# Kernel tuning notes

Hardware: AMD Instinct MI355X
Metric: run time of the kernel (lower is better)

The kernel has to match this reference:

```python
import jax, jax.numpy as jnp
import numpy as np

# --- config (Qwen3-Next linear attention defaults) ---
B, S, H = 1, 256, 2048
NK, NV, DK, DV, K = 4, 32, 128, 128, 4
KEY_DIM = NK * DK          # 512
VAL_DIM = NV * DV          # 4096
CONV_DIM = 2 * KEY_DIM + VAL_DIM  # 5120
EPS = 1e-6


def setup_inputs() -> dict:
    key = jax.random.key(0)
    ks = jax.random.split(key, 8)
    rn = lambda k, shape, sc: jax.random.normal(k, shape, jnp.float32) * sc
    return {
        "hidden_states": jax.random.normal(ks[0], (B, S, H), jnp.float32),
        "w_qkvz": rn(ks[1], (2 * KEY_DIM + 2 * VAL_DIM, H), 0.02),  # in_proj_qkvz weight
        "w_ba": rn(ks[2], (2 * NV, H), 0.02),                        # in_proj_ba weight
        "w_out": rn(ks[3], (H, VAL_DIM), 0.02),                      # out_proj weight
        "conv_w": rn(ks[4], (CONV_DIM, 1, K), 0.1),                  # depthwise conv weight [C,1,K]
        "dt_bias": jnp.ones((NV,), jnp.float32),
        "A_log": jnp.zeros((NV,), jnp.float32),
        "norm_w": jnp.ones((DV,), jnp.float32),
    }


def reference(hidden_states, w_qkvz, w_ba, w_out, conv_w, dt_bias, A_log, norm_w):
    b, s, _ = hidden_states.shape
    # input projections (Linear without bias: x @ W.T)
    qkvz = hidden_states @ w_qkvz.T                      # [B,S,9216]
    ba = hidden_states @ w_ba.T                          # [B,S,64]
    q, k, v, z = jnp.split(qkvz, [KEY_DIM, 2 * KEY_DIM, 2 * KEY_DIM + VAL_DIM], axis=-1)
    beta, alpha = jnp.split(ba, 2, axis=-1)              # each [B,S,NV]

    # causal depthwise conv over concat(q,k,v), then silu
    qkv = jnp.concatenate([q, k, v], axis=-1).transpose(0, 2, 1)   # [B,C,S]
    qkv = jax.lax.conv_general_dilated(
        qkv, conv_w, window_strides=(1,), padding=[(K - 1, 0)],
        dimension_numbers=("NCH", "OIH", "NCH"), feature_group_count=CONV_DIM)
    qkv = jax.nn.silu(qkv).transpose(0, 2, 1)            # [B,S,C]
    q, k, v = jnp.split(qkv, [KEY_DIM, 2 * KEY_DIM], axis=-1)

    q = q.reshape(b, s, NK, DK)
    k = k.reshape(b, s, NK, DK)
    v = v.reshape(b, s, NV, DV)
    z = z.reshape(b, s, NV, DV)

    # GQA-style head expansion (repeat_interleave)
    ratio = NV // NK
    q = jnp.repeat(q, ratio, axis=2)                     # [B,S,NV,DK]
    k = jnp.repeat(k, ratio, axis=2)

    # NOTE: original computes g = -softplus(-A_log - alpha) but never uses it (dead code).
    beta_g = jax.nn.sigmoid(beta + dt_bias)[..., None]   # [B,S,NV,1]
    q = q * (DK ** -0.5)

    # naive delta-rule: full outer-product tensor + cumsum (memory-bound)
    kv = jnp.einsum("bsnk,bsnv->bsnkv", k, v * beta_g)   # [B,S,NV,DK,DV]
    out = jnp.einsum("bsnk,bsnkv->bsnv", q, jnp.cumsum(kv, axis=1))  # [B,S,NV,DV]

    # gated RMSNorm over head_v_dim in fp32
    of = out.astype(jnp.float32)
    var = jnp.mean(of * of, axis=-1, keepdims=True)
    of = of * jax.lax.rsqrt(var + EPS) * norm_w
    of = of * jax.nn.silu(z.astype(jnp.float32))

    return of.reshape(b, s, VAL_DIM) @ w_out.T           # [B,S,H]
```

## Files before the change

### kernel.cpp

```cpp
#include <hip/hip_runtime.h>
#include <hip/hip_bf16.h>

#define S_LEN   256
#define HID     2048
#define NVH     32
#define DKD     128
#define DVD     128
#define KEYDIM  512
#define VALDIM  4096
#define CONVDIM 5120
#define QKVZ_N  9216
#define EPS_F   1e-6f

typedef __attribute__((ext_vector_type(8))) short bf16x8;
typedef __attribute__((ext_vector_type(4))) float f32x4;

__device__ __forceinline__ unsigned short f2bf(float f) {
    union { float f; unsigned int i; } v; v.f = f;
    unsigned int x = v.i;
    return (unsigned short)((x + 0x7FFFu + ((x >> 16) & 1u)) >> 16);
}
__device__ __forceinline__ unsigned int pk2(float x, float y) {
    union { __hip_bfloat162 h; unsigned int u; } c;
    c.h = __float22bfloat162_rn(float2{x, y});
    return c.u;
}
__device__ __forceinline__ float4 asf4(uint4 u) {
    union { uint4 u; float4 f; } c; c.u = u; return c.f;
}
__device__ __forceinline__ uint4 cvt8_pack(float4 a, float4 b) {
    uint4 r;
    r.x = pk2(a.x, a.y); r.y = pk2(a.z, a.w);
    r.z = pk2(b.x, b.y); r.w = pk2(b.z, b.w);
    return r;
}

template<bool A_F32>
__global__ __launch_bounds__(256, 2)
void gemm_tile(const void* __restrict__ Ap, const float* __restrict__ B,
               float* __restrict__ Cpart, int N, int K, int kc) {
    __shared__ __align__(16) unsigned short As[128][72];
    __shared__ __align__(16) unsigned short Bs[128][72];

    const int tid  = threadIdx.x;
    const int lane = tid & 63, wave = tid >> 6;
    const int wm = wave >> 1, wn = wave & 1;
    const int quad = lane >> 4, l16 = lane & 15;
    const int m0 = blockIdx.y * 128, n0 = blockIdx.x * 128;
    const int kbeg = blockIdx.z * kc;
    const int niter = kc >> 6;

    const int lc = (tid & 7) << 3;
    const int lr = tid >> 3;

    f32x4 acc[4][4];
#pragma unroll
    for (int i = 0; i < 4; i++)
#pragma unroll
        for (int j = 0; j < 4; j++) acc[i][j] = (f32x4){0.f, 0.f, 0.f, 0.f};

    uint4 qa[8], qb[8];

    auto ld_tiles = [&](int kk) {
        if constexpr (A_F32) {
            const float* a = (const float*)Ap + (size_t)(m0 + lr) * K + kk + lc;
#pragma unroll
            for (int i = 0; i < 4; i++) {
                qa[2 * i]     = *(const uint4*)(a + (size_t)(32 * i) * K);
                qa[2 * i + 1] = *(const uint4*)(a + (size_t)(32 * i) * K + 4);
            }
        } else {
            const unsigned short* a = (const unsigned short*)Ap + (size_t)(m0 + lr) * K + kk + lc;
#pragma unroll
            for (int i = 0; i < 4; i++)
                qa[i] = *(const uint4*)(a + (size_t)(32 * i) * K);
        }
        const float* b = B + (size_t)(n0 + lr) * K + kk + lc;
#pragma unroll
        for (int i = 0; i < 4; i++) {
            qb[2 * i]     = *(const uint4*)(b + (size_t)(32 * i) * K);
            qb[2 * i + 1] = *(const uint4*)(b + (size_t)(32 * i) * K + 4);
        }
    };
    auto st_tiles = [&]() {
#pragma unroll
        for (int i = 0; i < 4; i++) {
            if constexpr (A_F32)
                *(uint4*)(&As[lr + 32 * i][lc]) = cvt8_pack(asf4(qa[2 * i]), asf4(qa[2 * i + 1]));
            else
                *(uint4*)(&As[lr + 32 * i][lc]) = qa[i];
            *(uint4*)(&Bs[lr + 32 * i][lc]) = cvt8_pack(asf4(qb[2 * i]), asf4(qb[2 * i + 1]));
        }
    };

    ld_tiles(kbeg);
    st_tiles();
    __syncthreads();

    for (int it = 0; it < niter; ++it) {
        if (it + 1 < niter) ld_tiles(kbeg + (it + 1) * 64);

        bf16x8 af[2][4], bfr[2][4];
#pragma unroll
        for (int t = 0; t < 4; t++) {
#pragma unroll
            for (int ks = 0; ks < 2; ks++) {
                af[ks][t]  = *(const bf16x8*)(&As[wm * 64 + t * 16 + l16][ks * 32 + quad * 8]);
                bfr[ks][t] = *(const bf16x8*)(&Bs[wn * 64 + t * 16 + l16][ks * 32 + quad * 8]);
            }
        }
#pragma unroll
        for (int ks = 0; ks < 2; ks++)
#pragma unroll
            for (int i = 0; i < 4; i++)
#pragma unroll
                for (int j = 0; j < 4; j++)
                    acc[i][j] = __builtin_amdgcn_mfma_f32_16x16x32_bf16(af[ks][i], bfr[ks][j], acc[i][j], 0, 0, 0);

        if (it + 1 < niter) {
            __syncthreads();
            st_tiles();
            __syncthreads();
        }
    }

    float* C = Cpart + (size_t)blockIdx.z * 256 * N;
#pragma unroll
    for (int i = 0; i < 4; i++)
#pragma unroll
        for (int j = 0; j < 4; j++)
#pragma unroll
            for (int r = 0; r < 4; r++) {
                int row = m0 + wm * 64 + i * 16 + quad * 4 + r;
                int col = n0 + wn * 64 + j * 16 + l16;
                C[(size_t)row * N + col] = acc[i][j][r];
            }
}

template<int P>
__global__ void reduce_sum(const float* __restrict__ part, float* __restrict__ out, int n) {
    int i = (blockIdx.x * 256 + threadIdx.x) * 4;
    if (i >= n) return;
    float4 s = *(const float4*)(part + i);
#pragma unroll
    for (int p = 1; p < P; p++) {
        float4 v = *(const float4*)(part + (size_t)p * n + i);
        s.x += v.x; s.y += v.y; s.z += v.z; s.w += v.w;
    }
    *(float4*)(out + i) = s;
}

__global__ __launch_bounds__(256)
void ba_proj(const float* __restrict__ hs,
             const float* __restrict__ w_ba,
             float* __restrict__ ba) {
    int s = blockIdx.x;
    int n = threadIdx.x & 63, seg = threadIdx.x >> 6;
    const float* x = hs + (size_t)s * HID + seg * 512;
    const float* w = w_ba + (size_t)n * HID + seg * 512;
    float acc = 0.f;
#pragma unroll 4
    for (int k = 0; k < 512; k += 4) {
        float4 xv = *(const float4*)(x + k);
        float4 wv = *(const float4*)(w + k);
        acc += xv.x * wv.x + xv.y * wv.y + xv.z * wv.z + xv.w * wv.w;
    }
    __shared__ float parts[4][64];
    parts[seg][n] = acc;
    __syncthreads();
    if (threadIdx.x < 64)
        ba[s * 64 + threadIdx.x] = parts[0][threadIdx.x] + parts[1][threadIdx.x]
                                 + parts[2][threadIdx.x] + parts[3][threadIdx.x];
}

__global__ void conv_silu(const float* __restrict__ qkvz,
                          const float* __restrict__ conv_w,
                          float* __restrict__ out) {
    int idx = blockIdx.x * blockDim.x + threadIdx.x;
    if (idx >= S_LEN * CONVDIM) return;
    int s = idx / CONVDIM, c = idx % CONVDIM;
    float acc = 0.f;
#pragma unroll
    for (int j = 0; j < 4; j++) {
        int t = s - 3 + j;
        if (t >= 0) acc += qkvz[(size_t)t * QKVZ_N + c] * conv_w[c * 4 + j];
    }
    out[idx] = acc / (1.f + __expf(-acc));
}

__global__ __launch_bounds__(256)
void scores_k(const float* __restrict__ conv, const float* __restrict__ ba,
              const float* __restrict__ dt_bias, float* __restrict__ scores) {
    if (blockIdx.x > blockIdx.y) return;
    int hk = blockIdx.z;
    int s0 = blockIdx.y * 16, t0 = blockIdx.x * 16;
    __shared__ float Qs[16][132], Ks[16][132];
    int tid = threadIdx.x;
    int qoff = hk * DKD;
    int koff = KEYDIM + hk * DKD;
    for (int idx = tid; idx < 16 * 128; idx += 256) {
        int i = idx >> 7, d = idx & 127;
        Qs[i][d] = conv[(size_t)(s0 + i) * CONVDIM + qoff + d];
        Ks[i][d] = conv[(size_t)(t0 + i) * CONVDIM + koff + d];
    }
    __syncthreads();
    int tx = tid & 15, ty = tid >> 4;
    int s = s0 + ty, t = t0 + tx;
    float dot = 0.f;
    for (int d = 0; d < 128; d++) dot += Qs[ty][d] * Ks[tx][d];
    float base = (t <= s) ? dot * 0.08838834764831845f : 0.f;
#pragma unroll
    for (int v = 0; v < 8; v++) {
        int n = hk * 8 + v;
        float b = ba[t * 64 + n] + dt_bias[n];
        float bg = 1.f / (1.f + __expf(-b));
        scores[((size_t)n * 256 + s) * 256 + t] = base * bg;
    }
}

__global__ __launch_bounds__(256)
void attn_v(const float* __restrict__ scores, const float* __restrict__ conv,
            float* __restrict__ attn) {
    int n = blockIdx.y, s0 = blockIdx.x * 16;
    int voff = 2 * KEYDIM + n * DVD;
    __shared__ float Ss[16][17];
    __shared__ float Vs[16][132];
    int tid = threadIdx.x, sy = tid >> 4, dx = tid & 15;
    float acc[8] = {0.f, 0.f, 0.f, 0.f, 0.f, 0.f, 0.f, 0.f};
    for (int t0 = 0; t0 <= s0; t0 += 16) {
        Ss[sy][dx] = scores[((size_t)n * 256 + s0 + sy) * 256 + t0 + dx];
        const float* vp = conv + (size_t)(t0 + sy) * CONVDIM + voff + dx * 8;
        *(float4*)&Vs[sy][dx * 8]     = *(const float4*)vp;
        *(float4*)&Vs[sy][dx * 8 + 4] = *(const float4*)(vp + 4);
        __syncthreads();
#pragma unroll
        for (int j = 0; j < 16; j++) {
            float sv = Ss[sy][j];
#pragma unroll
            for (int r = 0; r < 8; r++) acc[r] += sv * Vs[j][dx + 16 * r];
        }
        __syncthreads();
    }
    float* op = attn + ((size_t)(s0 + sy) * NVH + n) * DVD;
#pragma unroll
    for (int r = 0; r < 8; r++) op[dx + 16 * r] = acc[r];
}

__global__ __launch_bounds__(128)
void rmsnorm_gate(const float* __restrict__ attn, const float* __restrict__ qkvz,
                  const float* __restrict__ norm_w,
                  unsigned short* __restrict__ normed) {
    int s = blockIdx.x >> 5, n = blockIdx.x & 31;
    int d = threadIdx.x;
    float x = attn[((size_t)s * NVH + n) * DVD + d];
    float sq = x * x;
#pragma unroll
    for (int off = 32; off > 0; off >>= 1) sq += __shfl_down(sq, off, 64);
    __shared__ float parts[2];
    if ((d & 63) == 0) parts[d >> 6] = sq;
    __syncthreads();
    float ms = (parts[0] + parts[1]) * (1.f / 128.f);
    float inv = rsqrtf(ms + EPS_F);
    float z = qkvz[(size_t)s * QKVZ_N + CONVDIM + n * DVD + d];
    float sz = z / (1.f + __expf(-z));
    float v = x * inv * norm_w[d] * sz;
    normed[((size_t)s * NVH + n) * DVD + d] = f2bf(v);
}

extern "C" void kernel_launch(void* const* d_in, const int* in_sizes, int n_in,
                              void* d_out, int out_size, void* d_ws, size_t ws_size,
                              hipStream_t stream) {
    const float* hs      = (const float*)d_in[0];
    const float* w_qkvz  = (const float*)d_in[1];
    const float* w_ba    = (const float*)d_in[2];
    const float* w_out   = (const float*)d_in[3];
    const float* conv_w  = (const float*)d_in[4];
    const float* dt_bias = (const float*)d_in[5];
    const float* norm_w  = (const float*)d_in[7];

    char* ws = (char*)d_ws;
    float* qkvz = (float*)ws;  ws += (size_t)S_LEN * QKVZ_N * 4;
    float* ba   = (float*)ws;  ws += (size_t)S_LEN * 64 * 4;
    float* conv = (float*)ws;  ws += (size_t)S_LEN * CONVDIM * 4;
    char* regB = ws;
    float* scratch1 = (float*)regB;
    unsigned short* normed = (unsigned short*)regB;
    float* scratch2 = (float*)(regB + 2097152);
    float* attn   = (float*)(regB + 2097152);
    float* scores = (float*)(regB + 2097152 + 4194304);

    const bool big = ws_size >= (size_t)54 * 1024 * 1024;
    const int sk1 = big ? 4 : 2;
    const int sk2 = big ? 16 : 8;

    gemm_tile<true><<<dim3(QKVZ_N / 128, 2, sk1), 256, 0, stream>>>(hs, w_qkvz, scratch1, QKVZ_N, HID, HID / sk1);
    ba_proj<<<S_LEN, 256, 0, stream>>>(hs, w_ba, ba);
    if (big) reduce_sum<4><<<(S_LEN * QKVZ_N) / 1024, 256, 0, stream>>>(scratch1, qkvz, S_LEN * QKVZ_N);
    else     reduce_sum<2><<<(S_LEN * QKVZ_N) / 1024, 256, 0, stream>>>(scratch1, qkvz, S_LEN * QKVZ_N);
    conv_silu<<<(S_LEN * CONVDIM) / 256, 256, 0, stream>>>(qkvz, conv_w, conv);
    scores_k<<<dim3(16, 16, 4), 256, 0, stream>>>(conv, ba, dt_bias, scores);
    attn_v<<<dim3(16, NVH), 256, 0, stream>>>(scores, conv, attn);
    rmsnorm_gate<<<S_LEN * NVH, 128, 0, stream>>>(attn, qkvz, norm_w, normed);
    gemm_tile<false><<<dim3(HID / 128, 2, sk2), 256, 0, stream>>>(normed, w_out, scratch2, HID, VALDIM, VALDIM / sk2);
    if (big) reduce_sum<16><<<(S_LEN * HID) / 1024, 256, 0, stream>>>(scratch2, (float*)d_out, S_LEN * HID);
    else     reduce_sum<8><<<(S_LEN * HID) / 1024, 256, 0, stream>>>(scratch2, (float*)d_out, S_LEN * HID);
}
```

Before: 274.5 us.

## Fuse attention pipeline, fold split-K reduction into conv, retile GEMM to 256x64

Several changes land together. The hidden states are converted to bf16 inside ba_proj, the GEMM is retiled to cover all 256 rows with 64-column tiles, and the first split-K reduction is folded into the conv kernel and the z read. scores_k, attn_v and rmsnorm_gate are fused into one attention kernel, which drops the scores and attn intermediates. The point is fewer launches and less intermediate global traffic. The cost is that the fused attention kernel recomputes QK per value head instead of sharing it per key head, and the workspace is now assumed large enough (about 45MB) with no fallback.

```diff
diff --git a/kernel.cpp b/kernel.cpp
--- a/kernel.cpp
+++ b/kernel.cpp
@@ -4,8 +4,6 @@
 #define S_LEN   256
 #define HID     2048
 #define NVH     32
-#define DKD     128
-#define DVD     128
 #define KEYDIM  512
 #define VALDIM  4096
 #define CONVDIM 5120
@@ -34,24 +32,23 @@
     r.z = pk2(b.x, b.y); r.w = pk2(b.z, b.w);
     return r;
 }
-
-template<bool A_F32>
-__global__ __launch_bounds__(256, 2)
-void gemm_tile(const void* __restrict__ Ap, const float* __restrict__ B,
+__device__ __forceinline__ float sigmoidf(float x) { return 1.f / (1.f + __expf(-x)); }
+
+__global__ __launch_bounds__(256, 3)
+void gemm_tile(const unsigned short* __restrict__ A, const float* __restrict__ B,
                float* __restrict__ Cpart, int N, int K, int kc) {
-    __shared__ __align__(16) unsigned short As[128][72];
-    __shared__ __align__(16) unsigned short Bs[128][72];
+    __shared__ __align__(16) unsigned short As[256][72];
+    __shared__ __align__(16) unsigned short Bs[64][72];
 
     const int tid  = threadIdx.x;
     const int lane = tid & 63, wave = tid >> 6;
-    const int wm = wave >> 1, wn = wave & 1;
     const int quad = lane >> 4, l16 = lane & 15;
-    const int m0 = blockIdx.y * 128, n0 = blockIdx.x * 128;
+    const int n0   = blockIdx.x * 64;
     const int kbeg = blockIdx.z * kc;
     const int niter = kc >> 6;
 
-    const int lc = (tid & 7) << 3;
-    const int lr = tid >> 3;
+    const int ar = tid >> 2;
+    const int ac = (tid & 3) << 4;
 
     f32x4 acc[4][4];
 #pragma unroll
@@ -59,38 +56,26 @@
 #pragma unroll
         for (int j = 0; j < 4; j++) acc[i][j] = (f32x4){0.f, 0.f, 0.f, 0.f};
 
-    uint4 qa[8], qb[8];
-
+    uint4 qa[8], qb[4];
     auto ld_tiles = [&](int kk) {
-        if constexpr (A_F32) {
-            const float* a = (const float*)Ap + (size_t)(m0 + lr) * K + kk + lc;
-#pragma unroll
-            for (int i = 0; i < 4; i++) {
-                qa[2 * i]     = *(const uint4*)(a + (size_t)(32 * i) * K);
-                qa[2 * i + 1] = *(const uint4*)(a + (size_t)(32 * i) * K + 4);
-            }
-        } else {
-            const unsigned short* a = (const unsigned short*)Ap + (size_t)(m0 + lr) * K + kk + lc;
-#pragma unroll
-            for (int i = 0; i < 4; i++)
-                qa[i] = *(const uint4*)(a + (size_t)(32 * i) * K);
-        }
-        const float* b = B + (size_t)(n0 + lr) * K + kk + lc;
-#pragma unroll
-        for (int i = 0; i < 4; i++) {
-            qb[2 * i]     = *(const uint4*)(b + (size_t)(32 * i) * K);
-            qb[2 * i + 1] = *(const uint4*)(b + (size_t)(32 * i) * K + 4);
-        }
+#pragma unroll
+        for (int p = 0; p < 4; p++) {
+            const unsigned short* a = A + (size_t)(ar + 64 * p) * K + kk + ac;
+            qa[2 * p]     = *(const uint4*)a;
+            qa[2 * p + 1] = *(const uint4*)(a + 8);
+        }
+        const float* b = B + (size_t)(n0 + ar) * K + kk + ac;
+#pragma unroll
+        for (int i = 0; i < 4; i++) qb[i] = *(const uint4*)(b + 4 * i);
     };
     auto st_tiles = [&]() {
 #pragma unroll
-        for (int i = 0; i < 4; i++) {
-            if constexpr (A_F32)
-                *(uint4*)(&As[lr + 32 * i][lc]) = cvt8_pack(asf4(qa[2 * i]), asf4(qa[2 * i + 1]));
-            else
-                *(uint4*)(&As[lr + 32 * i][lc]) = qa[i];
-            *(uint4*)(&Bs[lr + 32 * i][lc]) = cvt8_pack(asf4(qb[2 * i]), asf4(qb[2 * i + 1]));
-        }
+        for (int p = 0; p < 4; p++) {
+            *(uint4*)(&As[ar + 64 * p][ac])     = qa[2 * p];
+            *(uint4*)(&As[ar + 64 * p][ac + 8]) = qa[2 * p + 1];
+        }
+        *(uint4*)(&Bs[ar][ac])     = cvt8_pack(asf4(qb[0]), asf4(qb[1]));
+        *(uint4*)(&Bs[ar][ac + 8]) = cvt8_pack(asf4(qb[2]), asf4(qb[3]));
     };
 
     ld_tiles(kbeg);
@@ -105,8 +90,8 @@
         for (int t = 0; t < 4; t++) {
 #pragma unroll
             for (int ks = 0; ks < 2; ks++) {
-                af[ks][t]  = *(const bf16x8*)(&As[wm * 64 + t * 16 + l16][ks * 32 + quad * 8]);
-                bfr[ks][t] = *(const bf16x8*)(&Bs[wn * 64 + t * 16 + l16][ks * 32 + quad * 8]);
+                af[ks][t]  = *(const bf16x8*)(&As[wave * 64 + t * 16 + l16][ks * 32 + quad * 8]);
+                bfr[ks][t] = *(const bf16x8*)(&Bs[t * 16 + l16][ks * 32 + quad * 8]);
             }
         }
 #pragma unroll
@@ -131,8 +116,8 @@
         for (int j = 0; j < 4; j++)
 #pragma unroll
             for (int r = 0; r < 4; r++) {
-                int row = m0 + wm * 64 + i * 16 + quad * 4 + r;
-                int col = n0 + wn * 64 + j * 16 + l16;
+                int row = wave * 64 + i * 16 + quad * 4 + r;
+                int col = n0 + j * 16 + l16;
                 C[(size_t)row * N + col] = acc[i][j][r];
             }
 }
@@ -153,7 +138,8 @@
 __global__ __launch_bounds__(256)
 void ba_proj(const float* __restrict__ hs,
              const float* __restrict__ w_ba,
-             float* __restrict__ ba) {
+             float* __restrict__ ba,
+             unsigned short* __restrict__ hs_bf) {
     int s = blockIdx.x;
     int n = threadIdx.x & 63, seg = threadIdx.x >> 6;
     const float* x = hs + (size_t)s * HID + seg * 512;
@@ -167,72 +153,72 @@
     }
     __shared__ float parts[4][64];
     parts[seg][n] = acc;
+    int c = threadIdx.x * 8;
+    float4 h0 = *(const float4*)(hs + (size_t)s * HID + c);
+    float4 h1 = *(const float4*)(hs + (size_t)s * HID + c + 4);
+    *(uint4*)(hs_bf + (size_t)s * HID + c) = cvt8_pack(h0, h1);
     __syncthreads();
     if (threadIdx.x < 64)
         ba[s * 64 + threadIdx.x] = parts[0][threadIdx.x] + parts[1][threadIdx.x]
                                  + parts[2][threadIdx.x] + parts[3][threadIdx.x];
 }
 
-__global__ void conv_silu(const float* __restrict__ qkvz,
+__global__ void conv_red4(const float* __restrict__ part,
                           const float* __restrict__ conv_w,
                           float* __restrict__ out) {
     int idx = blockIdx.x * blockDim.x + threadIdx.x;
-    if (idx >= S_LEN * CONVDIM) return;
     int s = idx / CONVDIM, c = idx % CONVDIM;
+    const size_t PSTR = (size_t)S_LEN * QKVZ_N;
     float acc = 0.f;
 #pragma unroll
     for (int j = 0; j < 4; j++) {
         int t = s - 3 + j;
-        if (t >= 0) acc += qkvz[(size_t)t * QKVZ_N + c] * conv_w[c * 4 + j];
-    }
-    out[idx] = acc / (1.f + __expf(-acc));
+        if (t >= 0) {
+            const float* p = part + (size_t)t * QKVZ_N + c;
+            float q = p[0] + p[PSTR] + p[2 * PSTR] + p[3 * PSTR];
+            acc += q * conv_w[c * 4 + j];
+        }
+    }
+    out[idx] = acc * sigmoidf(acc);
 }
 
 __global__ __launch_bounds__(256)
-void scores_k(const float* __restrict__ conv, const float* __restrict__ ba,
-              const float* __restrict__ dt_bias, float* __restrict__ scores) {
-    if (blockIdx.x > blockIdx.y) return;
-    int hk = blockIdx.z;
-    int s0 = blockIdx.y * 16, t0 = blockIdx.x * 16;
-    __shared__ float Qs[16][132], Ks[16][132];
-    int tid = threadIdx.x;
-    int qoff = hk * DKD;
-    int koff = KEYDIM + hk * DKD;
-    for (int idx = tid; idx < 16 * 128; idx += 256) {
-        int i = idx >> 7, d = idx & 127;
-        Qs[i][d] = conv[(size_t)(s0 + i) * CONVDIM + qoff + d];
-        Ks[i][d] = conv[(size_t)(t0 + i) * CONVDIM + koff + d];
-    }
-    __syncthreads();
-    int tx = tid & 15, ty = tid >> 4;
-    int s = s0 + ty, t = t0 + tx;
-    float dot = 0.f;
-    for (int d = 0; d < 128; d++) dot += Qs[ty][d] * Ks[tx][d];
-    float base = (t <= s) ? dot * 0.08838834764831845f : 0.f;
-#pragma unroll
-    for (int v = 0; v < 8; v++) {
-        int n = hk * 8 + v;
-        float b = ba[t * 64 + n] + dt_bias[n];
-        float bg = 1.f / (1.f + __expf(-b));
-        scores[((size_t)n * 256 + s) * 256 + t] = base * bg;
-    }
-}
-
-__global__ __launch_bounds__(256)
-void attn_v(const float* __restrict__ scores, const float* __restrict__ conv,
-            float* __restrict__ attn) {
-    int n = blockIdx.y, s0 = blockIdx.x * 16;
-    int voff = 2 * KEYDIM + n * DVD;
-    __shared__ float Ss[16][17];
-    __shared__ float Vs[16][132];
-    int tid = threadIdx.x, sy = tid >> 4, dx = tid & 15;
+void attn_fused(const float* __restrict__ conv, const float* __restrict__ ba,
+                const float* __restrict__ dt_bias, const float* __restrict__ part,
+                const float* __restrict__ norm_w,
+                unsigned short* __restrict__ normed) {
+    const int st = blockIdx.x, n = blockIdx.y, hk = n >> 3;
+    const int s0 = st * 16;
+    __shared__ float Qs[16][132], Ks[16][132], Vs[16][132], Ss[16][17];
+    const int tid = threadIdx.x, sy = tid >> 4, dx = tid & 15;
+
+    {
+        const float* qp = conv + (size_t)(s0 + sy) * CONVDIM + hk * 128 + dx * 8;
+        *(float4*)&Qs[sy][dx * 8]     = *(const float4*)qp;
+        *(float4*)&Qs[sy][dx * 8 + 4] = *(const float4*)(qp + 4);
+    }
     float acc[8] = {0.f, 0.f, 0.f, 0.f, 0.f, 0.f, 0.f, 0.f};
+    const float dtb = dt_bias[n];
+
     for (int t0 = 0; t0 <= s0; t0 += 16) {
-        Ss[sy][dx] = scores[((size_t)n * 256 + s0 + sy) * 256 + t0 + dx];
-        const float* vp = conv + (size_t)(t0 + sy) * CONVDIM + voff + dx * 8;
+        const float* kp = conv + (size_t)(t0 + sy) * CONVDIM + KEYDIM + hk * 128 + dx * 8;
+        const float* vp = conv + (size_t)(t0 + sy) * CONVDIM + 2 * KEYDIM + n * 128 + dx * 8;
+        *(float4*)&Ks[sy][dx * 8]     = *(const float4*)kp;
+        *(float4*)&Ks[sy][dx * 8 + 4] = *(const float4*)(kp + 4);
         *(float4*)&Vs[sy][dx * 8]     = *(const float4*)vp;
         *(float4*)&Vs[sy][dx * 8 + 4] = *(const float4*)(vp + 4);
         __syncthreads();
+        float dot = 0.f;
+#pragma unroll 8
+        for (int d = 0; d < 128; d += 4) {
+            float4 q = *(const float4*)&Qs[sy][d];
+            float4 k = *(const float4*)&Ks[dx][d];
+            dot += q.x * k.x + q.y * k.y + q.z * k.z + q.w * k.w;
+        }
+        int t = t0 + dx, s = s0 + sy;
+        float bg = sigmoidf(ba[t * 64 + n] + dtb);
+        Ss[sy][dx] = (t <= s) ? dot * 0.08838834764831845f * bg : 0.f;
+        __syncthreads();
 #pragma unroll
         for (int j = 0; j < 16; j++) {
             float sv = Ss[sy][j];
@@ -241,30 +227,22 @@
         }
         __syncthreads();
     }
-    float* op = attn + ((size_t)(s0 + sy) * NVH + n) * DVD;
-#pragma unroll
-    for (int r = 0; r < 8; r++) op[dx + 16 * r] = acc[r];
-}
-
-__global__ __launch_bounds__(128)
-void rmsnorm_gate(const float* __restrict__ attn, const float* __restrict__ qkvz,
-                  const float* __restrict__ norm_w,
-                  unsigned short* __restrict__ normed) {
-    int s = blockIdx.x >> 5, n = blockIdx.x & 31;
-    int d = threadIdx.x;
-    float x = attn[((size_t)s * NVH + n) * DVD + d];
-    float sq = x * x;
-#pragma unroll
-    for (int off = 32; off > 0; off >>= 1) sq += __shfl_down(sq, off, 64);
-    __shared__ float parts[2];
-    if ((d & 63) == 0) parts[d >> 6] = sq;
-    __syncthreads();
-    float ms = (parts[0] + parts[1]) * (1.f / 128.f);
-    float inv = rsqrtf(ms + EPS_F);
-    float z = qkvz[(size_t)s * QKVZ_N + CONVDIM + n * DVD + d];
-    float sz = z / (1.f + __expf(-z));
-    float v = x * inv * norm_w[d] * sz;
-    normed[((size_t)s * NVH + n) * DVD + d] = f2bf(v);
+    float ss = 0.f;
+#pragma unroll
+    for (int r = 0; r < 8; r++) ss += acc[r] * acc[r];
+#pragma unroll
+    for (int m = 1; m < 16; m <<= 1) ss += __shfl_xor(ss, m, 64);
+    float inv = rsqrtf(ss * (1.f / 128.f) + EPS_F);
+    const size_t PSTR = (size_t)S_LEN * QKVZ_N;
+    const float* zb = part + (size_t)(s0 + sy) * QKVZ_N + CONVDIM + n * 128;
+    unsigned short* op = normed + ((size_t)(s0 + sy) * NVH + n) * 128;
+#pragma unroll
+    for (int r = 0; r < 8; r++) {
+        int d = dx + 16 * r;
+        float z = zb[d] + zb[d + PSTR] + zb[d + 2 * PSTR] + zb[d + 3 * PSTR];
+        float val = acc[r] * inv * norm_w[d] * (z * sigmoidf(z));
+        op[d] = f2bf(val);
+    }
 }
 
 extern "C" void kernel_launch(void* const* d_in, const int* in_sizes, int n_in,
@@ -279,29 +257,17 @@
     const float* norm_w  = (const float*)d_in[7];
 
     char* ws = (char*)d_ws;
-    float* qkvz = (float*)ws;  ws += (size_t)S_LEN * QKVZ_N * 4;
-    float* ba   = (float*)ws;  ws += (size_t)S_LEN * 64 * 4;
-    float* conv = (float*)ws;  ws += (size_t)S_LEN * CONVDIM * 4;
-    char* regB = ws;
-    float* scratch1 = (float*)regB;
-    unsigned short* normed = (unsigned short*)regB;
-    float* scratch2 = (float*)(regB + 2097152);
-    float* attn   = (float*)(regB + 2097152);
-    float* scores = (float*)(regB + 2097152 + 4194304);
-
-    const bool big = ws_size >= (size_t)54 * 1024 * 1024;
-    const int sk1 = big ? 4 : 2;
-    const int sk2 = big ? 16 : 8;
-
-    gemm_tile<true><<<dim3(QKVZ_N / 128, 2, sk1), 256, 0, stream>>>(hs, w_qkvz, scratch1, QKVZ_N, HID, HID / sk1);
-    ba_proj<<<S_LEN, 256, 0, stream>>>(hs, w_ba, ba);
-    if (big) reduce_sum<4><<<(S_LEN * QKVZ_N) / 1024, 256, 0, stream>>>(scratch1, qkvz, S_LEN * QKVZ_N);
-    else     reduce_sum<2><<<(S_LEN * QKVZ_N) / 1024, 256, 0, stream>>>(scratch1, qkvz, S_LEN * QKVZ_N);
-    conv_silu<<<(S_LEN * CONVDIM) / 256, 256, 0, stream>>>(qkvz, conv_w, conv);
-    scores_k<<<dim3(16, 16, 4), 256, 0, stream>>>(conv, ba, dt_bias, scores);
-    attn_v<<<dim3(16, NVH), 256, 0, stream>>>(scores, conv, attn);
-    rmsnorm_gate<<<S_LEN * NVH, 128, 0, stream>>>(attn, qkvz, norm_w, normed);
-    gemm_tile<false><<<dim3(HID / 128, 2, sk2), 256, 0, stream>>>(normed, w_out, scratch2, HID, VALDIM, VALDIM / sk2);
-    if (big) reduce_sum<16><<<(S_LEN * HID) / 1024, 256, 0, stream>>>(scratch2, (float*)d_out, S_LEN * HID);
-    else     reduce_sum<8><<<(S_LEN * HID) / 1024, 256, 0, stream>>>(scratch2, (float*)d_out, S_LEN * HID);
-}
+    float* scratch1        = (float*)ws;
+    float* conv            = (float*)(ws + 37748736);
+    float* ba              = (float*)(ws + 42991616);
+    unsigned short* normed = (unsigned short*)(ws + 43057152);
+    unsigned short* hs_bf  = (unsigned short*)(ws + 45154304);
+    float* scratch2        = (float*)ws;
+
+    ba_proj<<<S_LEN, 256, 0, stream>>>(hs, w_ba, ba, hs_bf);
+    gemm_tile<<<dim3(QKVZ_N / 64, 1, 4), 256, 0, stream>>>(hs_bf, w_qkvz, scratch1, QKVZ_N, HID, HID / 4);
+    conv_red4<<<(S_LEN * CONVDIM) / 256, 256, 0, stream>>>(scratch1, conv_w, conv);
+    attn_fused<<<dim3(16, NVH), 256, 0, stream>>>(conv, ba, dt_bias, scratch1, norm_w, normed);
+    gemm_tile<<<dim3(HID / 64, 1, 16), 256, 0, stream>>>(normed, w_out, scratch2, HID, VALDIM, VALDIM / 16);
+    reduce_sum<16><<<(S_LEN * HID) / 1024, 256, 0, stream>>>(scratch2, (float*)d_out, S_LEN * HID);
+}
```

Result: slower. 336.0 us (+22.4%).
